# Kernel tuning notes

Hardware: AMD Instinct MI355X
Metric: run time of the kernel (lower is better)

## Reference

```python
import jax, jax.numpy as jnp
import numpy as np

B, S, D = 2, 2048, 1024
H, HD = 16, 64

def setup_inputs() -> dict:
    key = jax.random.key(0)
    k1, k2, k3, k4 = jax.random.split(key, 4)
    inputs = jax.random.normal(k1, (B, S, D), dtype=jnp.float32)
    scale = 1.0 / np.sqrt(D)
    Wq = jax.random.normal(k2, (D, H * HD), dtype=jnp.float32) * scale
    Wk = jax.random.normal(k3, (D, H * HD), dtype=jnp.float32) * scale
    Wv = jax.random.normal(k4, (D, H * HD), dtype=jnp.float32) * scale
    return {"inputs": inputs, "Wq": Wq, "Wk": Wk, "Wv": Wv}

def _split_heads(x):
    # [B,S,H*HD] -> [B,H,S,HD]; tf.split along last axis == reshape then transpose
    b, s, _ = x.shape
    return x.reshape(b, s, H, HD).transpose(0, 2, 1, 3)

def reference(inputs, Wq, Wk, Wv):
    q = _split_heads(inputs @ Wq)  # [B,H,S,HD]
    k = _split_heads(inputs @ Wk)
    v = _split_heads(inputs @ Wv)
    scores = jnp.einsum("bhsd,bhtd->bhst", q, k) / jnp.sqrt(jnp.float32(HD))
    attn = jax.nn.softmax(scores, axis=-1)  # [B,H,S,S]
    out = jnp.einsum("bhst,bhtd->bhsd", attn, v)  # [B,H,S,HD]
    # concat heads back: [B,S,H*HD]
    return out.transpose(0, 2, 1, 3).reshape(inputs.shape[0], inputs.shape[1], H * HD)
```

## Files before the change

### kernel.cpp

```cpp
#include <hip/hip_runtime.h>

typedef __attribute__((ext_vector_type(8))) short short8;
typedef __attribute__((ext_vector_type(4))) float f32x4;
typedef __attribute__((ext_vector_type(16))) float f32x16;

#define B_  2
#define S_  2048
#define D_  1024
#define H_  16
#define HD_ 64
#define M_  (B_*S_)
#define N_  (H_*HD_)
#define HSZ ((size_t)B_*H_*S_*HD_)
#define BHS_ (B_*H_*S_)

#define QSCALE 0.18033688011112042f

__device__ __forceinline__ unsigned short f2bf(float f) {
  unsigned int u = __float_as_uint(f);
  u += 0x7fffu + ((u >> 16) & 1u);
  return (unsigned short)(u >> 16);
}

__device__ __forceinline__ unsigned int cvt_pk_bf16(float lo, float hi) {
  unsigned int r;
  asm("v_cvt_pk_bf16_f32 %0, %1, %2" : "=v"(r) : "v"(lo), "v"(hi));
  return r;
}

__device__ __forceinline__ float exp2_fast(float x) {
  float r;
  asm("v_exp_f32 %0, %1" : "=v"(r) : "v"(x));
  return r;
}

__device__ __forceinline__ void gll16(const void* g, void* l) {
  __builtin_amdgcn_global_load_lds(
      (const __attribute__((address_space(1))) void*)g,
      (__attribute__((address_space(3))) void*)l, 16, 0, 0);
}

__global__ void cvt_x_kernel(const float* __restrict__ x, unsigned short* __restrict__ xb) {
  int i = blockIdx.x * blockDim.x + threadIdx.x;
  float4 v = reinterpret_cast<const float4*>(x)[i];
  ushort4 o;
  o.x = f2bf(v.x); o.y = f2bf(v.y); o.z = f2bf(v.z); o.w = f2bf(v.w);
  reinterpret_cast<ushort4*>(xb)[i] = o;
}

__global__ void cvt_w_transpose_kernel(const float* __restrict__ w0, const float* __restrict__ w1,
                                       const float* __restrict__ w2, unsigned short* __restrict__ wt) {
  __shared__ float tile[32][33];
  const float* w = blockIdx.z == 0 ? w0 : (blockIdx.z == 1 ? w1 : w2);
  unsigned short* o = wt + (size_t)blockIdx.z * D_ * N_;
  int kbase = blockIdx.y * 32, nbase = blockIdx.x * 32;
#pragma unroll
  for (int i = 0; i < 4; i++)
    tile[threadIdx.y + i*8][threadIdx.x] =
        w[(size_t)(kbase + threadIdx.y + i*8) * N_ + nbase + threadIdx.x];
  __syncthreads();
#pragma unroll
  for (int i = 0; i < 4; i++)
    o[(size_t)(nbase + threadIdx.y + i*8) * D_ + kbase + threadIdx.x] =
        f2bf(tile[threadIdx.x][threadIdx.y + i*8]);
}

__global__ __launch_bounds__(256) void qkv_gemm_kernel(const unsigned short* __restrict__ xb,
                                                       const unsigned short* __restrict__ wt,
                                                       unsigned short* __restrict__ qkv) {
  __shared__ __align__(16) unsigned short As[128 * 64];
  __shared__ __align__(16) unsigned short Bs[128 * 64];
  const unsigned short* w = wt + (size_t)blockIdx.z * D_ * N_;
  unsigned short* out = qkv + (size_t)blockIdx.z * HSZ;
  int lane = threadIdx.x & 63, wave = threadIdx.x >> 6;
  int lr = lane & 15, lk = lane >> 4;
  int mblk = blockIdx.y * 128, nblk = blockIdx.x * 128;
  int wm = (wave >> 1) * 64, wn = (wave & 1) * 64;

  int srow0 = wave * 32 + (lane >> 3);
  int scol = lane & 7;
  f32x4 acc[4][4] = {};

  for (int kk = 0; kk < D_; kk += 64) {
    __syncthreads();
#pragma unroll
    for (int it = 0; it < 4; it++) {
      int row = srow0 + it * 8;
      int ce = (scol ^ (row & 7)) * 8;
      gll16(xb + (size_t)(mblk + row) * D_ + kk + ce,
            (void*)(As + (size_t)(wave * 4 + it) * 512));
      gll16(w  + (size_t)(nblk + row) * D_ + kk + ce,
            (void*)(Bs + (size_t)(wave * 4 + it) * 512));
    }
    __syncthreads();

    short8 a[2][4], b[2][4];
#pragma unroll
    for (int i = 0; i < 4; i++) {
      int row = wm + i * 16 + lr;
      const char* rp = (const char*)As + row * 128;
#pragma unroll
      for (int ks = 0; ks < 2; ks++)
        a[ks][i] = *reinterpret_cast<const short8*>(rp + ((((ks*4 + lk) ^ (row & 7))) << 4));
    }
#pragma unroll
    for (int j = 0; j < 4; j++) {
      int row = wn + j * 16 + lr;
      const char* rp = (const char*)Bs + row * 128;
#pragma unroll
      for (int ks = 0; ks < 2; ks++)
        b[ks][j] = *reinterpret_cast<const short8*>(rp + ((((ks*4 + lk) ^ (row & 7))) << 4));
    }
#pragma unroll
    for (int ks = 0; ks < 2; ks++)
#pragma unroll
      for (int i = 0; i < 4; i++)
#pragma unroll
        for (int j = 0; j < 4; j++)
          acc[i][j] = __builtin_amdgcn_mfma_f32_16x16x32_bf16(a[ks][i], b[ks][j], acc[i][j], 0, 0, 0);
  }

  if (blockIdx.z == 2) {
#pragma unroll
    for (int i = 0; i < 4; i++) {
      int m0 = mblk + wm + i*16 + lk*4;
      int bb = m0 >> 11, s0 = m0 & (S_-1);
#pragma unroll
      for (int j = 0; j < 4; j++) {
        int n = nblk + wn + j*16 + lr;
        int h = n >> 6, d = n & (HD_-1);
        ushort4 pk;
        pk.x = f2bf(acc[i][j][0]); pk.y = f2bf(acc[i][j][1]);
        pk.z = f2bf(acc[i][j][2]); pk.w = f2bf(acc[i][j][3]);
        *reinterpret_cast<ushort4*>(out + ((size_t)(bb*H_ + h)*HD_ + d)*S_ + s0) = pk;
      }
    }
  } else {
    float qs = (blockIdx.z == 0) ? QSCALE : 1.0f;
#pragma unroll
    for (int i = 0; i < 4; i++)
#pragma unroll
      for (int j = 0; j < 4; j++)
#pragma unroll
        for (int r = 0; r < 4; r++) {
          int m = mblk + wm + i*16 + lk*4 + r;
          int n = nblk + wn + j*16 + lr;
          int bb = m >> 11, s = m & (S_-1), h = n >> 6, d = n & (HD_-1);
          out[(((size_t)bb * H_ + h) * S_ + s) * HD_ + d] = f2bf(acc[i][j][r] * qs);
        }
  }
}

__global__ __launch_bounds__(256, 2) void attn_kernel(const unsigned short* __restrict__ qkv,
                                                      float* __restrict__ Opart,
                                                      float* __restrict__ ML) {
  int hid = blockIdx.x;
  int wrk = (hid & 7) * 64 + (hid >> 3);
  int bh = wrk >> 4, qt2 = (wrk >> 1) & 7, half = wrk & 1;

  const unsigned short* Q  = qkv +            (size_t)bh * S_ * HD_;
  const unsigned short* K  = qkv + HSZ   +    (size_t)bh * S_ * HD_;
  const unsigned short* Vt = qkv + 2*HSZ +    (size_t)bh * HD_ * S_;
  int lane = threadIdx.x & 63, wave = threadIdx.x >> 6;
  int ql = lane & 31, hi = lane >> 5;
  int qbase = qt2 * 256 + wave * 64;
  int tid = threadIdx.x;
  int kv0 = half * (S_/2);

  __shared__ __align__(16) unsigned short Ks[2][64 * 64];
  __shared__ __align__(16) unsigned short Vs[2][64 * 64];

#define STAGE(b, kc) do {                                                        \
    _Pragma("unroll")                                                            \
    for (int it = 0; it < 2; it++) {                                             \
      int ci = it * 256 + tid;                                                   \
      int rr = ci >> 3, cc = ci & 7;                                             \
      int ce = (cc ^ (rr & 7) ^ ((rr >> 3) & 7)) * 8;                            \
      gll16(K  + (size_t)((kc) + rr) * HD_ + ce, (void*)(Ks[b] + (size_t)ci*8)); \
      gll16(Vt + (size_t)rr * S_ + (kc) + ce,    (void*)(Vs[b] + (size_t)ci*8)); \
    }                                                                            \
  } while (0)

  short8 qf[2][4];
#pragma unroll
  for (int qt = 0; qt < 2; qt++)
#pragma unroll
    for (int ds = 0; ds < 4; ds++)
      qf[qt][ds] = *reinterpret_cast<const short8*>(
          Q + (size_t)(qbase + qt*32 + ql) * HD_ + ds*16 + hi*8);

  unsigned short o0v = (ql < 16) ? 0x3F80 : 0;
  short8 ones0, ones1;
#pragma unroll
  for (int i = 0; i < 8; i++) { ones0[i] = (short)o0v; ones1[i] = (short)(o0v ^ 0x3F80); }

  f32x16 oacc[2][2] = {};
  f32x16 lacc = {};
  float m0 = -INFINITY, m1 = -INFINITY;

  STAGE(0, kv0);

#pragma unroll 2
  for (int kt = 0; kt < S_/128; kt++) {
    int buf = kt & 1;
    __syncthreads();
    if (kt < S_/128 - 1) STAGE(buf^1, kv0 + (kt+1)*64);

    short8 kf[2][4];
#pragma unroll
    for (int kh = 0; kh < 2; kh++) {
      int row = kh*32 + ql;
      const char* rp = (const char*)Ks[buf] + row * 128;
      int sw = (row & 7) ^ ((row >> 3) & 7);
#pragma unroll
      for (int ds = 0; ds < 4; ds++)
        kf[kh][ds] = *reinterpret_cast<const short8*>(rp + (((ds*2 + hi) ^ sw) << 4));
    }
    f32x16 s0[2] = {}, s1[2] = {};
    __builtin_amdgcn_s_setprio(1);
#pragma unroll
    for (int kh = 0; kh < 2; kh++)
#pragma unroll
      for (int ds = 0; ds < 4; ds++) {
        s0[kh] = __builtin_amdgcn_mfma_f32_32x32x16_bf16(kf[kh][ds], qf[0][ds], s0[kh], 0, 0, 0);
        s1[kh] = __builtin_amdgcn_mfma_f32_32x32x16_bf16(kf[kh][ds], qf[1][ds], s1[kh], 0, 0, 0);
      }
    __builtin_amdgcn_s_setprio(0);

    {
      float tm[16];
#pragma unroll
      for (int r = 0; r < 16; r++) tm[r] = fmaxf(s0[0][r], s0[1][r]);
#pragma unroll
      for (int st = 8; st > 0; st >>= 1)
#pragma unroll
        for (int r = 0; r < st; r++) tm[r] = fmaxf(tm[r], tm[r + st]);
      float mx = fmaxf(tm[0], __shfl_xor(tm[0], 32));
      if (__any(mx - m0 > 8.0f)) {
        float mn = fmaxf(m0, mx);
        float c = exp2_fast(m0 - mn);
        m0 = mn;
#pragma unroll
        for (int r = 0; r < 8; r++) lacc[r] *= c;
#pragma unroll
        for (int dh = 0; dh < 2; dh++)
#pragma unroll
          for (int r = 0; r < 16; r++) oacc[0][dh][r] *= c;
      }
#pragma unroll
      for (int kh = 0; kh < 2; kh++)
#pragma unroll
        for (int r = 0; r < 16; r++) s0[kh][r] = exp2_fast(s0[kh][r] - m0);
    }
    {
      float tm[16];
#pragma unroll
      for (int r = 0; r < 16; r++) tm[r] = fmaxf(s1[0][r], s1[1][r]);
#pragma unroll
      for (int st = 8; st > 0; st >>= 1)
#pragma unroll
        for (int r = 0; r < st; r++) tm[r] = fmaxf(tm[r], tm[r + st]);
      float mx = fmaxf(tm[0], __shfl_xor(tm[0], 32));
      if (__any(mx - m1 > 8.0f)) {
        float mn = fmaxf(m1, mx);
        float c = exp2_fast(m1 - mn);
        m1 = mn;
#pragma unroll
        for (int r = 8; r < 16; r++) lacc[r] *= c;
#pragma unroll
        for (int dh = 0; dh < 2; dh++)
#pragma unroll
          for (int r = 0; r < 16; r++) oacc[1][dh][r] *= c;
      }
#pragma unroll
      for (int kh = 0; kh < 2; kh++)
#pragma unroll
        for (int r = 0; r < 16; r++) s1[kh][r] = exp2_fast(s1[kh][r] - m1);
    }

    short8 vf[4][2];
#pragma unroll
    for (int ks = 0; ks < 4; ks++) {
      int o = (ks & 1) * 8;
      int kh = ks >> 1;
      unsigned int w0 = cvt_pk_bf16(s0[kh][o+0], s0[kh][o+1]);
      unsigned int w1 = cvt_pk_bf16(s0[kh][o+2], s0[kh][o+3]);
      unsigned int w2 = cvt_pk_bf16(s0[kh][o+4], s0[kh][o+5]);
      unsigned int w3 = cvt_pk_bf16(s0[kh][o+6], s0[kh][o+7]);
      asm("v_permlane32_swap_b32 %0, %1" : "+v"(w0), "+v"(w2));
      asm("v_permlane32_swap_b32 %0, %1" : "+v"(w1), "+v"(w3));
      union { unsigned int u[4]; short8 v; } pf;
      pf.u[0] = w0; pf.u[1] = w1; pf.u[2] = w2; pf.u[3] = w3;
      __builtin_amdgcn_s_setprio(1);
      lacc = __builtin_amdgcn_mfma_f32_32x32x16_bf16(ones0, pf.v, lacc, 0, 0, 0);
#pragma unroll
      for (int dh = 0; dh < 2; dh++) {
        int row = dh*32 + ql;
        int sw = (row & 7) ^ ((row >> 3) & 7);
        vf[ks][dh] = *reinterpret_cast<const short8*>(
            (const char*)Vs[buf] + row * 128 + (((ks*2 + hi) ^ sw) << 4));
        oacc[0][dh] = __builtin_amdgcn_mfma_f32_32x32x16_bf16(vf[ks][dh], pf.v, oacc[0][dh], 0, 0, 0);
      }
      __builtin_amdgcn_s_setprio(0);
    }
#pragma unroll
    for (int ks = 0; ks < 4; ks++) {
      int o = (ks & 1) * 8;
      int kh = ks >> 1;
      unsigned int w0 = cvt_pk_bf16(s1[kh][o+0], s1[kh][o+1]);
      unsigned int w1 = cvt_pk_bf16(s1[kh][o+2], s1[kh][o+3]);
      unsigned int w2 = cvt_pk_bf16(s1[kh][o+4], s1[kh][o+5]);
      unsigned int w3 = cvt_pk_bf16(s1[kh][o+6], s1[kh][o+7]);
      asm("v_permlane32_swap_b32 %0, %1" : "+v"(w0), "+v"(w2));
      asm("v_permlane32_swap_b32 %0, %1" : "+v"(w1), "+v"(w3));
      union { unsigned int u[4]; short8 v; } pf;
      pf.u[0] = w0; pf.u[1] = w1; pf.u[2] = w2; pf.u[3] = w3;
      __builtin_amdgcn_s_setprio(1);
      lacc = __builtin_amdgcn_mfma_f32_32x32x16_bf16(ones1, pf.v, lacc, 0, 0, 0);
#pragma unroll
      for (int dh = 0; dh < 2; dh++)
        oacc[1][dh] = __builtin_amdgcn_mfma_f32_32x32x16_bf16(vf[ks][dh], pf.v, oacc[1][dh], 0, 0, 0);
      __builtin_amdgcn_s_setprio(0);
    }
  }

#pragma unroll
  for (int qt = 0; qt < 2; qt++) {
    float l = lacc[qt * 8];
    int s = qbase + qt*32 + ql;
    size_t prow = (size_t)half * BHS_ + (size_t)bh * S_ + s;
    float* orow = Opart + prow * HD_;
#pragma unroll
    for (int dh = 0; dh < 2; dh++)
#pragma unroll
      for (int a = 0; a < 4; a++) {
        float4 vv;
        vv.x = oacc[qt][dh][a*4+0]; vv.y = oacc[qt][dh][a*4+1];
        vv.z = oacc[qt][dh][a*4+2]; vv.w = oacc[qt][dh][a*4+3];
        *reinterpret_cast<float4*>(orow + dh*32 + 8*a + 4*hi) = vv;
      }
    if (hi == 0) {
      float2 ml; ml.x = (qt == 0) ? m0 : m1; ml.y = l;
      reinterpret_cast<float2*>(ML)[prow] = ml;
    }
  }
#undef STAGE
}

__global__ __launch_bounds__(256) void combine_kernel(const float* __restrict__ Opart,
                                                      const float* __restrict__ ML,
                                                      float* __restrict__ out) {
  int idx = blockIdx.x * 256 + threadIdx.x;
  int row = idx >> 4;
  int dc = (idx & 15) * 4;
  float2 ml0 = reinterpret_cast<const float2*>(ML)[row];
  float2 ml1 = reinterpret_cast<const float2*>(ML)[BHS_ + row];
  float M = fmaxf(ml0.x, ml1.x);
  float w0 = exp2_fast(ml0.x - M), w1 = exp2_fast(ml1.x - M);
  float inv = 1.0f / (ml0.y * w0 + ml1.y * w1);
  float4 o0 = *reinterpret_cast<const float4*>(Opart + (size_t)row * HD_ + dc);
  float4 o1 = *reinterpret_cast<const float4*>(Opart + ((size_t)BHS_ + row) * HD_ + dc);
  float4 r;
  r.x = (o0.x*w0 + o1.x*w1) * inv; r.y = (o0.y*w0 + o1.y*w1) * inv;
  r.z = (o0.z*w0 + o1.z*w1) * inv; r.w = (o0.w*w0 + o1.w*w1) * inv;
  int bh = row >> 11, s = row & (S_-1);
  int b = bh >> 4, h = bh & (H_-1);
  *reinterpret_cast<float4*>(out + ((size_t)b * S_ + s) * N_ + h * HD_ + dc) = r;
}

extern "C" void kernel_launch(void* const* d_in, const int* in_sizes, int n_in,
                              void* d_out, int out_size, void* d_ws, size_t ws_size,
                              hipStream_t stream) {
  const float* X  = (const float*)d_in[0];
  const float* Wq = (const float*)d_in[1];
  const float* Wk = (const float*)d_in[2];
  const float* Wv = (const float*)d_in[3];
  float* out = (float*)d_out;

  unsigned short* Xb  = (unsigned short*)d_ws;
  unsigned short* Wt  = Xb + (size_t)M_ * D_;
  unsigned short* QKV = Wt + (size_t)3 * D_ * N_;
  float* Opart = (float*)(QKV + 3 * HSZ);
  float* ML    = Opart + (size_t)2 * BHS_ * HD_;

  cvt_x_kernel<<<(M_*D_)/(256*4), 256, 0, stream>>>(X, Xb);
  cvt_w_transpose_kernel<<<dim3(N_/32, D_/32, 3), dim3(32, 8), 0, stream>>>(Wq, Wk, Wv, Wt);
  qkv_gemm_kernel<<<dim3(N_/128, M_/128, 3), 256, 0, stream>>>(Xb, Wt, QKV);
  attn_kernel<<<(S_/256) * (B_*H_) * 2, 256, 0, stream>>>(QKV, Opart, ML);
  combine_kernel<<<(BHS_*16)/256, 256, 0, stream>>>(Opart, ML, out);
}
```

Baseline: 122.1 us.

## Fuse conversion kernels, deepen KV staging, drop ones-MFMA row sums, store fp16 partials

Merges the input and weight conversion kernels into one launch. In attention, the KV staging grows to four LDS buffers, loaded two tiles at a time with a barrier every other iteration. Row sums of the softmax are now done with VALU adds and a cross-lane shuffle instead of an extra MFMA against a ones matrix. The partial outputs are stored as fp16 to halve the write and read traffic into the combine kernel. This doubles LDS use per block, which may reduce occupancy, and adds fp16 rounding to the partial outputs.

```diff
diff --git a/kernel.cpp b/kernel.cpp
--- a/kernel.cpp
+++ b/kernel.cpp
@@ -1,4 +1,5 @@
 #include <hip/hip_runtime.h>
+#include <hip/hip_fp16.h>
 
 typedef __attribute__((ext_vector_type(8))) short short8;
 typedef __attribute__((ext_vector_type(4))) float f32x4;
@@ -40,29 +41,35 @@
       (__attribute__((address_space(3))) void*)l, 16, 0, 0);
 }
 
-__global__ void cvt_x_kernel(const float* __restrict__ x, unsigned short* __restrict__ xb) {
-  int i = blockIdx.x * blockDim.x + threadIdx.x;
-  float4 v = reinterpret_cast<const float4*>(x)[i];
-  ushort4 o;
-  o.x = f2bf(v.x); o.y = f2bf(v.y); o.z = f2bf(v.z); o.w = f2bf(v.w);
-  reinterpret_cast<ushort4*>(xb)[i] = o;
-}
-
-__global__ void cvt_w_transpose_kernel(const float* __restrict__ w0, const float* __restrict__ w1,
-                                       const float* __restrict__ w2, unsigned short* __restrict__ wt) {
+__global__ __launch_bounds__(256) void cvt_all_kernel(const float* __restrict__ x,
+                                                      const float* __restrict__ w0,
+                                                      const float* __restrict__ w1,
+                                                      const float* __restrict__ w2,
+                                                      unsigned short* __restrict__ xb,
+                                                      unsigned short* __restrict__ wt) {
   __shared__ float tile[32][33];
-  const float* w = blockIdx.z == 0 ? w0 : (blockIdx.z == 1 ? w1 : w2);
-  unsigned short* o = wt + (size_t)blockIdx.z * D_ * N_;
-  int kbase = blockIdx.y * 32, nbase = blockIdx.x * 32;
+  int bid = blockIdx.x;
+  if (bid < 4096) {
+    int i = bid * 256 + threadIdx.x;
+    float4 v = reinterpret_cast<const float4*>(x)[i];
+    ushort4 o;
+    o.x = f2bf(v.x); o.y = f2bf(v.y); o.z = f2bf(v.z); o.w = f2bf(v.w);
+    reinterpret_cast<ushort4*>(xb)[i] = o;
+    return;
+  }
+  int wid = bid - 4096;
+  int z = wid >> 10, rem = wid & 1023;
+  int nbase = (rem & 31) * 32, kbase = (rem >> 5) * 32;
+  int tx = threadIdx.x & 31, ty = threadIdx.x >> 5;
+  const float* w = z == 0 ? w0 : (z == 1 ? w1 : w2);
+  unsigned short* o = wt + (size_t)z * D_ * N_;
 #pragma unroll
   for (int i = 0; i < 4; i++)
-    tile[threadIdx.y + i*8][threadIdx.x] =
-        w[(size_t)(kbase + threadIdx.y + i*8) * N_ + nbase + threadIdx.x];
+    tile[ty + i*8][tx] = w[(size_t)(kbase + ty + i*8) * N_ + nbase + tx];
   __syncthreads();
 #pragma unroll
   for (int i = 0; i < 4; i++)
-    o[(size_t)(nbase + threadIdx.y + i*8) * D_ + kbase + threadIdx.x] =
-        f2bf(tile[threadIdx.x][threadIdx.y + i*8]);
+    o[(size_t)(nbase + ty + i*8) * D_ + kbase + tx] = f2bf(tile[tx][ty + i*8]);
 }
 
 __global__ __launch_bounds__(256) void qkv_gemm_kernel(const unsigned short* __restrict__ xb,
@@ -152,7 +159,7 @@
 }
 
 __global__ __launch_bounds__(256, 2) void attn_kernel(const unsigned short* __restrict__ qkv,
-                                                      float* __restrict__ Opart,
+                                                      __half* __restrict__ Opart,
                                                       float* __restrict__ ML) {
   int hid = blockIdx.x;
   int wrk = (hid & 7) * 64 + (hid >> 3);
@@ -167,8 +174,8 @@
   int tid = threadIdx.x;
   int kv0 = half * (S_/2);
 
-  __shared__ __align__(16) unsigned short Ks[2][64 * 64];
-  __shared__ __align__(16) unsigned short Vs[2][64 * 64];
+  __shared__ __align__(16) unsigned short Ks[4][64 * 64];
+  __shared__ __align__(16) unsigned short Vs[4][64 * 64];
 
 #define STAGE(b, kc) do {                                                        \
     _Pragma("unroll")                                                            \
@@ -189,22 +196,23 @@
       qf[qt][ds] = *reinterpret_cast<const short8*>(
           Q + (size_t)(qbase + qt*32 + ql) * HD_ + ds*16 + hi*8);
 
-  unsigned short o0v = (ql < 16) ? 0x3F80 : 0;
-  short8 ones0, ones1;
-#pragma unroll
-  for (int i = 0; i < 8; i++) { ones0[i] = (short)o0v; ones1[i] = (short)(o0v ^ 0x3F80); }
-
   f32x16 oacc[2][2] = {};
-  f32x16 lacc = {};
   float m0 = -INFINITY, m1 = -INFINITY;
+  float lsum0 = 0.f, lsum1 = 0.f;
 
   STAGE(0, kv0);
-
-#pragma unroll 2
-  for (int kt = 0; kt < S_/128; kt++) {
-    int buf = kt & 1;
-    __syncthreads();
-    if (kt < S_/128 - 1) STAGE(buf^1, kv0 + (kt+1)*64);
+  STAGE(1, kv0 + 64);
+
+#pragma unroll 4
+  for (int kt = 0; kt < 16; kt++) {
+    int buf = kt & 3;
+    if ((kt & 1) == 0) {
+      __syncthreads();
+      if (kt < 14) {
+        STAGE((kt + 2) & 3, kv0 + (kt + 2) * 64);
+        STAGE((kt + 3) & 3, kv0 + (kt + 3) * 64);
+      }
+    }
 
     short8 kf[2][4];
 #pragma unroll
@@ -228,11 +236,12 @@
     __builtin_amdgcn_s_setprio(0);
 
     {
-      float tm[16];
-#pragma unroll
-      for (int r = 0; r < 16; r++) tm[r] = fmaxf(s0[0][r], s0[1][r]);
-#pragma unroll
-      for (int st = 8; st > 0; st >>= 1)
+      float tm[8];
+#pragma unroll
+      for (int r = 0; r < 8; r++)
+        tm[r] = fmaxf(fmaxf(s0[0][r], s0[0][r+8]), fmaxf(s0[1][r], s0[1][r+8]));
+#pragma unroll
+      for (int st = 4; st > 0; st >>= 1)
 #pragma unroll
         for (int r = 0; r < st; r++) tm[r] = fmaxf(tm[r], tm[r + st]);
       float mx = fmaxf(tm[0], __shfl_xor(tm[0], 32));
@@ -240,8 +249,7 @@
         float mn = fmaxf(m0, mx);
         float c = exp2_fast(m0 - mn);
         m0 = mn;
-#pragma unroll
-        for (int r = 0; r < 8; r++) lacc[r] *= c;
+        lsum0 *= c;
 #pragma unroll
         for (int dh = 0; dh < 2; dh++)
 #pragma unroll
@@ -251,13 +259,23 @@
       for (int kh = 0; kh < 2; kh++)
 #pragma unroll
         for (int r = 0; r < 16; r++) s0[kh][r] = exp2_fast(s0[kh][r] - m0);
+      float ts[8];
+#pragma unroll
+      for (int r = 0; r < 8; r++)
+        ts[r] = (s0[0][r] + s0[0][r+8]) + (s0[1][r] + s0[1][r+8]);
+#pragma unroll
+      for (int st = 4; st > 0; st >>= 1)
+#pragma unroll
+        for (int r = 0; r < st; r++) ts[r] += ts[r + st];
+      lsum0 += ts[0] + __shfl_xor(ts[0], 32);
     }
     {
-      float tm[16];
-#pragma unroll
-      for (int r = 0; r < 16; r++) tm[r] = fmaxf(s1[0][r], s1[1][r]);
-#pragma unroll
-      for (int st = 8; st > 0; st >>= 1)
+      float tm[8];
+#pragma unroll
+      for (int r = 0; r < 8; r++)
+        tm[r] = fmaxf(fmaxf(s1[0][r], s1[0][r+8]), fmaxf(s1[1][r], s1[1][r+8]));
+#pragma unroll
+      for (int st = 4; st > 0; st >>= 1)
 #pragma unroll
         for (int r = 0; r < st; r++) tm[r] = fmaxf(tm[r], tm[r + st]);
       float mx = fmaxf(tm[0], __shfl_xor(tm[0], 32));
@@ -265,8 +283,7 @@
         float mn = fmaxf(m1, mx);
         float c = exp2_fast(m1 - mn);
         m1 = mn;
-#pragma unroll
-        for (int r = 8; r < 16; r++) lacc[r] *= c;
+        lsum1 *= c;
 #pragma unroll
         for (int dh = 0; dh < 2; dh++)
 #pragma unroll
@@ -276,6 +293,15 @@
       for (int kh = 0; kh < 2; kh++)
 #pragma unroll
         for (int r = 0; r < 16; r++) s1[kh][r] = exp2_fast(s1[kh][r] - m1);
+      float ts[8];
+#pragma unroll
+      for (int r = 0; r < 8; r++)
+        ts[r] = (s1[0][r] + s1[0][r+8]) + (s1[1][r] + s1[1][r+8]);
+#pragma unroll
+      for (int st = 4; st > 0; st >>= 1)
+#pragma unroll
+        for (int r = 0; r < st; r++) ts[r] += ts[r + st];
+      lsum1 += ts[0] + __shfl_xor(ts[0], 32);
     }
 
     short8 vf[4][2];
@@ -292,7 +318,6 @@
       union { unsigned int u[4]; short8 v; } pf;
       pf.u[0] = w0; pf.u[1] = w1; pf.u[2] = w2; pf.u[3] = w3;
       __builtin_amdgcn_s_setprio(1);
-      lacc = __builtin_amdgcn_mfma_f32_32x32x16_bf16(ones0, pf.v, lacc, 0, 0, 0);
 #pragma unroll
       for (int dh = 0; dh < 2; dh++) {
         int row = dh*32 + ql;
@@ -316,7 +341,6 @@
       union { unsigned int u[4]; short8 v; } pf;
       pf.u[0] = w0; pf.u[1] = w1; pf.u[2] = w2; pf.u[3] = w3;
       __builtin_amdgcn_s_setprio(1);
-      lacc = __builtin_amdgcn_mfma_f32_32x32x16_bf16(ones1, pf.v, lacc, 0, 0, 0);
 #pragma unroll
       for (int dh = 0; dh < 2; dh++)
         oacc[1][dh] = __builtin_amdgcn_mfma_f32_32x32x16_bf16(vf[ks][dh], pf.v, oacc[1][dh], 0, 0, 0);
@@ -326,46 +350,54 @@
 
 #pragma unroll
   for (int qt = 0; qt < 2; qt++) {
-    float l = lacc[qt * 8];
     int s = qbase + qt*32 + ql;
     size_t prow = (size_t)half * BHS_ + (size_t)bh * S_ + s;
-    float* orow = Opart + prow * HD_;
+    __half* orow = Opart + prow * HD_;
 #pragma unroll
     for (int dh = 0; dh < 2; dh++)
 #pragma unroll
       for (int a = 0; a < 4; a++) {
-        float4 vv;
-        vv.x = oacc[qt][dh][a*4+0]; vv.y = oacc[qt][dh][a*4+1];
-        vv.z = oacc[qt][dh][a*4+2]; vv.w = oacc[qt][dh][a*4+3];
-        *reinterpret_cast<float4*>(orow + dh*32 + 8*a + 4*hi) = vv;
+        union { __half2 h[2]; uint2 u; } pk;
+        pk.h[0] = __float22half2_rn(make_float2(oacc[qt][dh][a*4+0], oacc[qt][dh][a*4+1]));
+        pk.h[1] = __float22half2_rn(make_float2(oacc[qt][dh][a*4+2], oacc[qt][dh][a*4+3]));
+        *reinterpret_cast<uint2*>(orow + dh*32 + 8*a + 4*hi) = pk.u;
       }
     if (hi == 0) {
-      float2 ml; ml.x = (qt == 0) ? m0 : m1; ml.y = l;
+      float2 ml; ml.x = (qt == 0) ? m0 : m1; ml.y = (qt == 0) ? lsum0 : lsum1;
       reinterpret_cast<float2*>(ML)[prow] = ml;
     }
   }
 #undef STAGE
 }
 
-__global__ __launch_bounds__(256) void combine_kernel(const float* __restrict__ Opart,
+__global__ __launch_bounds__(256) void combine_kernel(const __half* __restrict__ Opart,
                                                       const float* __restrict__ ML,
                                                       float* __restrict__ out) {
   int idx = blockIdx.x * 256 + threadIdx.x;
-  int row = idx >> 4;
-  int dc = (idx & 15) * 4;
+  int row = idx >> 3;
+  int dc = (idx & 7) * 8;
   float2 ml0 = reinterpret_cast<const float2*>(ML)[row];
   float2 ml1 = reinterpret_cast<const float2*>(ML)[BHS_ + row];
   float M = fmaxf(ml0.x, ml1.x);
   float w0 = exp2_fast(ml0.x - M), w1 = exp2_fast(ml1.x - M);
   float inv = 1.0f / (ml0.y * w0 + ml1.y * w1);
-  float4 o0 = *reinterpret_cast<const float4*>(Opart + (size_t)row * HD_ + dc);
-  float4 o1 = *reinterpret_cast<const float4*>(Opart + ((size_t)BHS_ + row) * HD_ + dc);
-  float4 r;
-  r.x = (o0.x*w0 + o1.x*w1) * inv; r.y = (o0.y*w0 + o1.y*w1) * inv;
-  r.z = (o0.z*w0 + o1.z*w1) * inv; r.w = (o0.w*w0 + o1.w*w1) * inv;
+  const __half2* p0 = reinterpret_cast<const __half2*>(Opart + (size_t)row * HD_ + dc);
+  const __half2* p1 = reinterpret_cast<const __half2*>(Opart + ((size_t)BHS_ + row) * HD_ + dc);
+  float r[8];
+#pragma unroll
+  for (int i = 0; i < 4; i++) {
+    float2 a = __half22float2(p0[i]);
+    float2 b = __half22float2(p1[i]);
+    r[2*i+0] = (a.x*w0 + b.x*w1) * inv;
+    r[2*i+1] = (a.y*w0 + b.y*w1) * inv;
+  }
   int bh = row >> 11, s = row & (S_-1);
   int b = bh >> 4, h = bh & (H_-1);
-  *reinterpret_cast<float4*>(out + ((size_t)b * S_ + s) * N_ + h * HD_ + dc) = r;
+  float* po = out + ((size_t)b * S_ + s) * N_ + h * HD_ + dc;
+  float4 v0; v0.x = r[0]; v0.y = r[1]; v0.z = r[2]; v0.w = r[3];
+  float4 v1; v1.x = r[4]; v1.y = r[5]; v1.z = r[6]; v1.w = r[7];
+  *reinterpret_cast<float4*>(po)     = v0;
+  *reinterpret_cast<float4*>(po + 4) = v1;
 }
 
 extern "C" void kernel_launch(void* const* d_in, const int* in_sizes, int n_in,
@@ -380,12 +412,11 @@
   unsigned short* Xb  = (unsigned short*)d_ws;
   unsigned short* Wt  = Xb + (size_t)M_ * D_;
   unsigned short* QKV = Wt + (size_t)3 * D_ * N_;
-  float* Opart = (float*)(QKV + 3 * HSZ);
-  float* ML    = Opart + (size_t)2 * BHS_ * HD_;
-
-  cvt_x_kernel<<<(M_*D_)/(256*4), 256, 0, stream>>>(X, Xb);
-  cvt_w_transpose_kernel<<<dim3(N_/32, D_/32, 3), dim3(32, 8), 0, stream>>>(Wq, Wk, Wv, Wt);
+  __half* Opart = (__half*)(QKV + 3 * HSZ);
+  float* ML    = (float*)(Opart + (size_t)2 * BHS_ * HD_);
+
+  cvt_all_kernel<<<4096 + 3072, 256, 0, stream>>>(X, Wq, Wk, Wv, Xb, Wt);
   qkv_gemm_kernel<<<dim3(N_/128, M_/128, 3), 256, 0, stream>>>(Xb, Wt, QKV);
   attn_kernel<<<(S_/256) * (B_*H_) * 2, 256, 0, stream>>>(QKV, Opart, ML);
-  combine_kernel<<<(BHS_*16)/256, 256, 0, stream>>>(Opart, ML, out);
-}
+  combine_kernel<<<(BHS_*8)/256, 256, 0, stream>>>(Opart, ML, out);
+}
```

Measured after the change: 115.6 us. 1.06x faster.
